# Kernel optimization log

Hardware: AMD Instinct MI355X
Metric: run time of the kernel (lower is better)

The kernel has to match this reference:

```python
import jax, jax.numpy as jnp
import numpy as np

NUM_HEADS = 4
OUTPUT_DIM = 64


def setup_inputs() -> dict:
    key = jax.random.key(0)
    k1, k2, k3 = jax.random.split(key, 3)
    B, N, F = 8, 2048, 256
    features = jax.random.normal(k1, (B, N, F), dtype=jnp.float32)
    adj_matrix = jax.random.uniform(k2, (B, N, N), dtype=jnp.float32)
    # learned params (glorot-ish scale)
    kernel = jax.random.normal(k3, (F, OUTPUT_DIM * NUM_HEADS), dtype=jnp.float32) * (1.0 / np.sqrt(F))
    bias = jnp.zeros((OUTPUT_DIM * NUM_HEADS,), dtype=jnp.float32)
    return {"features": features, "adj_matrix": adj_matrix, "kernel": kernel, "bias": bias}


def reference(features, adj_matrix, kernel, bias):
    B, N, F = features.shape
    H, D = NUM_HEADS, OUTPUT_DIM
    Wh = jnp.matmul(features, kernel)                 # [B, N, H*D]
    Whh = Wh.reshape(B, N, H, D)                      # [B, N, H, D]
    # per-node, per-head score: inner product Wh1 @ Wh2 = ||Wh||^2
    e = jnp.sum(Whh * Whh, axis=-1)                   # [B, N, H]
    attention = jax.nn.softmax(e, axis=1)             # softmax over nodes
    attention = jnp.mean(attention, axis=2)           # head mean -> [B, N]
    # adjacency mask (broadcast column score over neighbors)
    A = attention[:, :, None] * adj_matrix            # [B, N, N]
    out = jnp.matmul(A, Wh) + bias                    # [B, N, H*D]
    return jax.nn.relu(out)
```

## Files before the change

kernel.cpp:

```cpp
#include <hip/hip_runtime.h>
#include <hip/hip_bf16.h>

#define BATCH 8
#define NNODE 2048
#define FDIM 256
#define HD 256
#define NH 4
#define MROWS (BATCH*NNODE)

typedef float f32x4 __attribute__((ext_vector_type(4)));
typedef short s16x8 __attribute__((ext_vector_type(8)));
typedef unsigned short ushort_t;

#define MFMA __builtin_amdgcn_mfma_f32_16x16x32_bf16
#define SCHED0() __builtin_amdgcn_sched_barrier(0)
#define SBAR() __builtin_amdgcn_s_barrier()

__device__ __forceinline__ ushort_t f2bf(float f) {
    unsigned u = __builtin_bit_cast(unsigned, f);
    u += 0x7fffu + ((u >> 16) & 1u);
    return (ushort_t)(u >> 16);
}
__device__ __forceinline__ void split2(float f, ushort_t& h, ushort_t& l) {
    unsigned u = __builtin_bit_cast(unsigned, f);
    h = (ushort_t)(u >> 16);
    float fh = __builtin_bit_cast(float, u & 0xffff0000u);
    float lo = f - fh;
    l = (ushort_t)(__builtin_bit_cast(unsigned, lo) >> 16);
}

#define GLOAD16(gp, lp) __builtin_amdgcn_global_load_lds( \
    (const __attribute__((address_space(1))) void*)(gp),  \
    (__attribute__((address_space(3))) void*)(lp), 16, 0, 0)

__global__ __launch_bounds__(256) void wprep_kernel(
    const float* __restrict__ Wm,
    ushort_t* __restrict__ wt_hi, ushort_t* __restrict__ wt_lo)
{
    const int nn = blockIdx.x, k = threadIdx.x;
    ushort_t h, l;
    split2(Wm[(size_t)k * HD + nn], h, l);
    wt_hi[nn * FDIM + k] = h;
    wt_lo[nn * FDIM + k] = l;
}

__global__ __launch_bounds__(256, 4) void gemm1_kernel(
    const float* __restrict__ features,
    const ushort_t* __restrict__ wt_hi,
    const ushort_t* __restrict__ wt_lo,
    ushort_t* __restrict__ WhT_hi,
    float* __restrict__ e_out)
{
    __shared__ __align__(16) ushort_t Ah[64 * 64];
    __shared__ __align__(16) ushort_t Al[64 * 64];
    __shared__ __align__(16) ushort_t Bh[64 * 64];
    __shared__ __align__(16) ushort_t Bl[64 * 64];
    __shared__ float red[64][2];

    const int tid = threadIdx.x, lane = tid & 63, w = tid >> 6;
    const int wr = w >> 1, wc = w & 1;
    const int row0 = blockIdx.x * 64;
    const int head = blockIdx.y;
    const int col0 = head * 64;

    const float* Ab = features + (size_t)row0 * FDIM;
    const ushort_t* Bhg = wt_hi + (size_t)col0 * FDIM;
    const ushort_t* Blg = wt_lo + (size_t)col0 * FDIM;

    const int sr0 = tid >> 3;
    const int sg8 = tid & 7;
    const int bc = (lane >> 3);
    const int bs = lane & 7;

    f32x4 ar[4];
    f32x4 acc[2][2];
    #pragma unroll
    for (int m = 0; m < 2; ++m)
        #pragma unroll
        for (int n = 0; n < 2; ++n) acc[m][n] = (f32x4)0.f;

    #define G1_LOADA(K0) do {                                                  \
        _Pragma("unroll")                                                      \
        for (int i = 0; i < 2; ++i) {                                          \
            const int r = sr0 + 32 * i;                                        \
            ar[2*i]   = *(const f32x4*)&Ab[(size_t)r * FDIM + (K0) + sg8 * 8]; \
            ar[2*i+1] = *(const f32x4*)&Ab[(size_t)r * FDIM + (K0) + sg8 * 8 + 4]; \
        }                                                                      \
    } while (0)

    #define G1_STAGEA() do {                                                   \
        _Pragma("unroll")                                                      \
        for (int i = 0; i < 2; ++i) {                                          \
            const int r = sr0 + 32 * i;                                        \
            s16x8 vh, vl; ushort_t hh, ll;                                     \
            _Pragma("unroll")                                                  \
            for (int j = 0; j < 4; ++j) {                                      \
                split2(ar[2*i][j], hh, ll);  vh[j] = (short)hh; vl[j] = (short)ll; \
            }                                                                  \
            _Pragma("unroll")                                                  \
            for (int j = 0; j < 4; ++j) {                                      \
                split2(ar[2*i+1][j], hh, ll); vh[4+j] = (short)hh; vl[4+j] = (short)ll; \
            }                                                                  \
            const int off = r * 64 + ((sg8 ^ (r & 7)) << 3);                   \
            *(s16x8*)&Ah[off] = vh; *(s16x8*)&Al[off] = vl;                    \
        }                                                                      \
    } while (0)

    #define G1_STAGEB(K0) do {                                                 \
        _Pragma("unroll")                                                      \
        for (int qq = 0; qq < 2; ++qq) {                                       \
            const int q = w + qq * 4;                                          \
            const int c = q * 8 + bc;                                          \
            const int g = bs ^ (c & 7);                                        \
            GLOAD16(&Bhg[(size_t)c * FDIM + (K0) + g * 8], &Bh[q * 512]);      \
            GLOAD16(&Blg[(size_t)c * FDIM + (K0) + g * 8], &Bl[q * 512]);      \
        }                                                                      \
    } while (0)

    G1_LOADA(0);
    for (int t = 0; t < 4; ++t) {
        G1_STAGEB(t * 64);
        G1_STAGEA();
        if (t < 3) G1_LOADA((t + 1) * 64);
        if (t < 3) { asm volatile("s_waitcnt lgkmcnt(0) vmcnt(4)" ::: "memory"); }
        else       { asm volatile("s_waitcnt lgkmcnt(0) vmcnt(0)" ::: "memory"); }
        SCHED0(); SBAR(); SCHED0();
        #pragma unroll
        for (int kh = 0; kh < 2; ++kh) {
            const int kg = kh * 4 + (lane >> 4);
            s16x8 afh[2], afl[2], bfh[2], bfl[2];
            #pragma unroll
            for (int m = 0; m < 2; ++m) {
                const int r = wr * 32 + m * 16 + (lane & 15);
                const int off = r * 64 + ((kg ^ (r & 7)) << 3);
                afh[m] = *(const s16x8*)&Ah[off];
                afl[m] = *(const s16x8*)&Al[off];
            }
            #pragma unroll
            for (int n = 0; n < 2; ++n) {
                const int c = wc * 32 + n * 16 + (lane & 15);
                const int off = c * 64 + ((kg ^ (c & 7)) << 3);
                bfh[n] = *(const s16x8*)&Bh[off];
                bfl[n] = *(const s16x8*)&Bl[off];
            }
            #pragma unroll
            for (int m = 0; m < 2; ++m)
                #pragma unroll
                for (int n = 0; n < 2; ++n) {
                    acc[m][n] = MFMA(afh[m], bfh[n], acc[m][n], 0, 0, 0);
                    acc[m][n] = MFMA(afh[m], bfl[n], acc[m][n], 0, 0, 0);
                    acc[m][n] = MFMA(afl[m], bfh[n], acc[m][n], 0, 0, 0);
                }
        }
        SCHED0(); SBAR(); SCHED0();
    }

    #pragma unroll
    for (int m = 0; m < 2; ++m)
        #pragma unroll
        for (int j = 0; j < 4; ++j) {
            float p = acc[m][0][j] * acc[m][0][j] + acc[m][1][j] * acc[m][1][j];
            p += __shfl_xor(p, 1, 64);
            p += __shfl_xor(p, 2, 64);
            p += __shfl_xor(p, 4, 64);
            p += __shfl_xor(p, 8, 64);
            if ((lane & 15) == 0)
                red[wr * 32 + m * 16 + (lane >> 4) * 4 + j][wc] = p;
        }

    __syncthreads();
    ushort_t* Th = Ah;
    #pragma unroll
    for (int m = 0; m < 2; ++m)
        #pragma unroll
        for (int n = 0; n < 2; ++n)
            #pragma unroll
            for (int j = 0; j < 4; ++j) {
                const int rr = wr * 32 + m * 16 + (lane >> 4) * 4 + j;
                const int cc = wc * 32 + n * 16 + (lane & 15);
                const int ad = cc * 64 + ((((rr >> 3) ^ (cc & 7))) << 3) + (rr & 7);
                Th[ad] = f2bf(acc[m][n][j]);
            }
    __syncthreads();

    if (tid < 64) {
        const int rg = row0 + tid;
        e_out[((size_t)((rg >> 11) * NH + head)) * NNODE + (rg & 2047)] =
            red[tid][0] + red[tid][1];
    }
    const int bb = row0 >> 11, node0 = row0 & 2047;
    {
        const int gid = tid + 256 * 0;
        #pragma unroll
        for (int i = 0; i < 2; ++i) {
            const int g2 = gid + 256 * i;
            const int c = g2 >> 3, gr = g2 & 7;
            const int ad = c * 64 + ((gr ^ (c & 7)) << 3);
            uint4 vh = *(const uint4*)&Th[ad];
            const size_t o = ((size_t)bb * HD + col0 + c) * NNODE + node0 + gr * 8;
            *(uint4*)&WhT_hi[o] = vh;
        }
    }
}

__global__ __launch_bounds__(256) void sm_kernel(
    const float* __restrict__ e, float* __restrict__ ms)
{
    __shared__ float red[8];
    const int bh = blockIdx.x, tid = threadIdx.x;
    const int lane = tid & 63, w = tid >> 6;
    const float* row = e + (size_t)bh * NNODE;
    float mx = -3.0e38f;
    for (int n = tid; n < NNODE; n += 256) mx = fmaxf(mx, row[n]);
    #pragma unroll
    for (int off = 32; off; off >>= 1) mx = fmaxf(mx, __shfl_xor(mx, off, 64));
    if (lane == 0) red[w] = mx;
    __syncthreads();
    mx = fmaxf(fmaxf(red[0], red[1]), fmaxf(red[2], red[3]));
    float s = 0.f;
    for (int n = tid; n < NNODE; n += 256) s += expf(row[n] - mx);
    #pragma unroll
    for (int off = 32; off; off >>= 1) s += __shfl_xor(s, off, 64);
    if (lane == 0) red[4 + w] = s;
    __syncthreads();
    if (tid == 0) {
        ms[bh * 2] = mx;
        ms[bh * 2 + 1] = 1.0f / (red[4] + red[5] + red[6] + red[7]);
    }
}

__global__ __launch_bounds__(256, 2) void gemm2_kernel(
    const float* __restrict__ adj,
    const ushort_t* __restrict__ WhT_hi,
    const float* __restrict__ e,
    const float* __restrict__ ms,
    const float* __restrict__ bias,
    float* __restrict__ out)
{
    __shared__ __align__(16) ushort_t Bh[4][64 * 64];

    const int tid = threadIdx.x, lane = tid & 63, w = tid >> 6;

    const int bid = blockIdx.x;
    const int wg = (bid & 7) * 64 + (bid >> 3);
    const int bx = wg & 15, by = (wg >> 4) & 3, b = wg >> 6;
    const int row0 = bx * 128, col0 = by * 64;

    const ushort_t* Bhg = WhT_hi + ((size_t)b * HD + col0) * NNODE;
    const float* pA = adj + (size_t)b * NNODE * NNODE
                    + (size_t)(row0 + w * 32 + (lane & 15)) * NNODE
                    + ((lane >> 4) * 8);

    const int bc = lane >> 3, bs = lane & 7;

    f32x4 arE[8], arO[8];
    s16x8 afh[2][2];
    f32x4 acc[2][4];
    #pragma unroll
    for (int m = 0; m < 2; ++m)
        #pragma unroll
        for (int n = 0; n < 4; ++n) acc[m][n] = (f32x4)0.f;

    #define G2_LOADA(AR, K0) do {                                               \
        _Pragma("unroll")                                                       \
        for (int m = 0; m < 2; ++m)                                             \
        _Pragma("unroll")                                                       \
        for (int ks = 0; ks < 2; ++ks) {                                        \
            AR[m*4+ks*2+0] = *(const f32x4*)&pA[(size_t)m * 16 * NNODE + (K0) + ks * 32]; \
            AR[m*4+ks*2+1] = *(const f32x4*)&pA[(size_t)m * 16 * NNODE + (K0) + ks * 32 + 4]; \
        }                                                                       \
    } while (0)

    #define G2_CONVERT(AR) do {                                                 \
        _Pragma("unroll")                                                       \
        for (int m = 0; m < 2; ++m)                                             \
        _Pragma("unroll")                                                       \
        for (int ks = 0; ks < 2; ++ks)                                          \
        _Pragma("unroll")                                                       \
        for (int h2 = 0; h2 < 2; ++h2)                                          \
        _Pragma("unroll")                                                       \
        for (int j = 0; j < 4; ++j)                                             \
            afh[m][ks][h2 * 4 + j] = (short)f2bf(AR[m*4+ks*2+h2][j]);           \
    } while (0)

    #define G2_STAGEB(BUF, K0) do {                                             \
        _Pragma("unroll")                                                       \
        for (int qq = 0; qq < 2; ++qq) {                                        \
            const int q = w + qq * 4;                                           \
            const int c = q * 8 + bc;                                           \
            const int g = bs ^ (c & 7);                                         \
            GLOAD16(&Bhg[(size_t)c * NNODE + (K0) + g * 8], &Bh[BUF][q * 512]); \
        }                                                                       \
    } while (0)

    #define G2_COMPUTE(BUF) do {                                                \
        _Pragma("unroll")                                                       \
        for (int ks = 0; ks < 2; ++ks) {                                        \
            const int kg = ks * 4 + (lane >> 4);                                \
            s16x8 bfh[4];                                                       \
            _Pragma("unroll")                                                   \
            for (int n = 0; n < 4; ++n) {                                       \
                const int c = n * 16 + (lane & 15);                             \
                const int off = c * 64 + ((kg ^ (c & 7)) << 3);                 \
                bfh[n] = *(const s16x8*)&Bh[BUF][off];                          \
            }                                                                   \
            __builtin_amdgcn_s_setprio(1);                                      \
            _Pragma("unroll")                                                   \
            for (int m = 0; m < 2; ++m)                                         \
            _Pragma("unroll")                                                   \
            for (int n = 0; n < 4; ++n)                                         \
                acc[m][n] = MFMA(afh[m][ks], bfh[n], acc[m][n], 0, 0, 0);       \
            __builtin_amdgcn_s_setprio(0);                                      \
        }                                                                       \
    } while (0)

    #define G2_TILE(AR, CBUF, SBUF, KC, DO_STAGE) do {                          \
        if (DO_STAGE) G2_STAGEB(SBUF, (KC) + 128);                              \
        G2_CONVERT(AR);                                                         \
        if (DO_STAGE) G2_LOADA(AR, (KC) + 128);                                 \
        asm volatile("s_waitcnt vmcnt(20)" ::: "memory");                       \
        SCHED0(); SBAR(); SCHED0();                                             \
        G2_COMPUTE(CBUF);                                                       \
    } while (0)

    G2_STAGEB(0, 0);
    G2_LOADA(arE, 0);
    G2_STAGEB(1, 64);
    G2_LOADA(arO, 64);

    #pragma unroll 1
    for (int t = 0; t < 28; t += 4) {
        G2_TILE(arE, 0, 2, t * 64, true);
        G2_TILE(arO, 1, 3, (t + 1) * 64, true);
        G2_TILE(arE, 2, 0, (t + 2) * 64, true);
        G2_TILE(arO, 3, 1, (t + 3) * 64, true);
    }
    G2_TILE(arE, 0, 2, 28 * 64, true);
    G2_TILE(arO, 1, 3, 29 * 64, true);
    G2_TILE(arE, 2, 0, 30 * 64, false);
    G2_TILE(arO, 3, 0, 31 * 64, false);

    float msm[NH], msi[NH];
    #pragma unroll
    for (int h = 0; h < NH; ++h) {
        msm[h] = ms[(b * NH + h) * 2];
        msi[h] = ms[(b * NH + h) * 2 + 1];
    }
    float rowatt[2][4];
    #pragma unroll
    for (int m = 0; m < 2; ++m)
        #pragma unroll
        for (int j = 0; j < 4; ++j) {
            const int row = row0 + w * 32 + m * 16 + (lane >> 4) * 4 + j;
            float a = 0.f;
            #pragma unroll
            for (int h = 0; h < NH; ++h)
                a += expf(e[((size_t)b * NH + h) * NNODE + row] - msm[h]) * msi[h];
            rowatt[m][j] = 0.25f * a;
        }
    #pragma unroll
    for (int n = 0; n < 4; ++n) {
        const int c = col0 + n * 16 + (lane & 15);
        const float bv = bias[c];
        #pragma unroll
        for (int m = 0; m < 2; ++m)
            #pragma unroll
            for (int j = 0; j < 4; ++j) {
                const int row = row0 + w * 32 + m * 16 + (lane >> 4) * 4 + j;
                out[((size_t)b * NNODE + row) * HD + c] =
                    fmaxf(fmaf(acc[m][n][j], rowatt[m][j], bv), 0.f);
            }
    }
}

extern "C" void kernel_launch(void* const* d_in, const int* in_sizes, int n_in,
                              void* d_out, int out_size, void* d_ws, size_t ws_size,
                              hipStream_t stream) {
    const float* features = (const float*)d_in[0];
    const float* adj      = (const float*)d_in[1];
    const float* Wm       = (const float*)d_in[2];
    const float* bias     = (const float*)d_in[3];
    float* out = (float*)d_out;

    ushort_t* WhT_hi = (ushort_t*)d_ws;
    ushort_t* wt_hi  = WhT_hi + (size_t)BATCH * HD * NNODE;
    ushort_t* wt_lo  = wt_hi + FDIM * HD;
    float* e  = (float*)(wt_lo + FDIM * HD);
    float* ms = e + (size_t)BATCH * NH * NNODE;

    wprep_kernel<<<HD, 256, 0, stream>>>(Wm, wt_hi, wt_lo);
    gemm1_kernel<<<dim3(MROWS / 64, NH), 256, 0, stream>>>(
        features, wt_hi, wt_lo, WhT_hi, e);
    sm_kernel<<<BATCH * NH, 256, 0, stream>>>(e, ms);
    gemm2_kernel<<<512, 256, 0, stream>>>(
        adj, WhT_hi, e, ms, bias, out);
}
```

Before: 265.4 us.

## Give each wave a private B buffer in gemm2 to drop block barriers

Each wave of gemm2 now stages the full 64x64 B tile into its own private double-buffered LDS slot and then reads only that slot. The s_barrier between stages goes away, replaced by per-wave waitcnt on vmcnt and lgkmcnt, and the pipeline changes from four shared buffers to two private ones. In exchange, global B traffic per block rises fourfold (each wave loads all 64 columns), LDS use doubles to 64KB, and the prefetch distance for B shrinks. A small cleanup to the epilogue loop of the first kernel is also included.

```diff
diff --git a/kernel.cpp b/kernel.cpp
--- a/kernel.cpp
+++ b/kernel.cpp
@@ -189,17 +189,14 @@
             red[tid][0] + red[tid][1];
     }
     const int bb = row0 >> 11, node0 = row0 & 2047;
-    {
-        const int gid = tid + 256 * 0;
-        #pragma unroll
-        for (int i = 0; i < 2; ++i) {
-            const int g2 = gid + 256 * i;
-            const int c = g2 >> 3, gr = g2 & 7;
-            const int ad = c * 64 + ((gr ^ (c & 7)) << 3);
-            uint4 vh = *(const uint4*)&Th[ad];
-            const size_t o = ((size_t)bb * HD + col0 + c) * NNODE + node0 + gr * 8;
-            *(uint4*)&WhT_hi[o] = vh;
-        }
+    #pragma unroll
+    for (int i = 0; i < 2; ++i) {
+        const int g2 = tid + 256 * i;
+        const int c = g2 >> 3, gr = g2 & 7;
+        const int ad = c * 64 + ((gr ^ (c & 7)) << 3);
+        uint4 vh = *(const uint4*)&Th[ad];
+        const size_t o = ((size_t)bb * HD + col0 + c) * NNODE + node0 + gr * 8;
+        *(uint4*)&WhT_hi[o] = vh;
     }
 }
 
@@ -237,7 +234,7 @@
     const float* __restrict__ bias,
     float* __restrict__ out)
 {
-    __shared__ __align__(16) ushort_t Bh[4][64 * 64];
+    __shared__ __align__(16) ushort_t Bh[4][2][64 * 64];
 
     const int tid = threadIdx.x, lane = tid & 63, w = tid >> 6;
 
@@ -251,7 +248,10 @@
                     + (size_t)(row0 + w * 32 + (lane & 15)) * NNODE
                     + ((lane >> 4) * 8);
 
-    const int bc = lane >> 3, bs = lane & 7;
+    const int scol = lane >> 3;
+    const int sgr  = (lane & 7) ^ scol;
+    ushort_t* myB0 = &Bh[w][0][0];
+    ushort_t* myB1 = &Bh[w][1][0];
 
     f32x4 arE[8], arO[8];
     s16x8 afh[2][2];
@@ -283,17 +283,15 @@
             afh[m][ks][h2 * 4 + j] = (short)f2bf(AR[m*4+ks*2+h2][j]);           \
     } while (0)
 
-    #define G2_STAGEB(BUF, K0) do {                                             \
-        _Pragma("unroll")                                                       \
-        for (int qq = 0; qq < 2; ++qq) {                                        \
-            const int q = w + qq * 4;                                           \
-            const int c = q * 8 + bc;                                           \
-            const int g = bs ^ (c & 7);                                         \
-            GLOAD16(&Bhg[(size_t)c * NNODE + (K0) + g * 8], &Bh[BUF][q * 512]); \
+    #define G2_STAGEB(LB, K0) do {                                              \
+        _Pragma("unroll")                                                       \
+        for (int i = 0; i < 8; ++i) {                                           \
+            const int c = i * 8 + scol;                                         \
+            GLOAD16(&Bhg[(size_t)c * NNODE + (K0) + sgr * 8], (LB) + i * 512);  \
         }                                                                       \
     } while (0)
 
-    #define G2_COMPUTE(BUF) do {                                                \
+    #define G2_COMPUTE(LB) do {                                                 \
         _Pragma("unroll")                                                       \
         for (int ks = 0; ks < 2; ++ks) {                                        \
             const int kg = ks * 4 + (lane >> 4);                                \
@@ -302,7 +300,7 @@
             for (int n = 0; n < 4; ++n) {                                       \
                 const int c = n * 16 + (lane & 15);                             \
                 const int off = c * 64 + ((kg ^ (c & 7)) << 3);                 \
-                bfh[n] = *(const s16x8*)&Bh[BUF][off];                          \
+                bfh[n] = *(const s16x8*)&(LB)[off];                             \
             }                                                                   \
             __builtin_amdgcn_s_setprio(1);                                      \
             _Pragma("unroll")                                                   \
@@ -314,31 +312,51 @@
         }                                                                       \
     } while (0)
 
-    #define G2_TILE(AR, CBUF, SBUF, KC, DO_STAGE) do {                          \
-        if (DO_STAGE) G2_STAGEB(SBUF, (KC) + 128);                              \
-        G2_CONVERT(AR);                                                         \
-        if (DO_STAGE) G2_LOADA(AR, (KC) + 128);                                 \
-        asm volatile("s_waitcnt vmcnt(20)" ::: "memory");                       \
-        SCHED0(); SBAR(); SCHED0();                                             \
-        G2_COMPUTE(CBUF);                                                       \
-    } while (0)
-
-    G2_STAGEB(0, 0);
+    #define LGK0() asm volatile("s_waitcnt lgkmcnt(0)" ::: "memory")
+
+    G2_STAGEB(myB0, 0);
+    SCHED0();
     G2_LOADA(arE, 0);
-    G2_STAGEB(1, 64);
+    SCHED0();
     G2_LOADA(arO, 64);
+    SCHED0();
 
     #pragma unroll 1
-    for (int t = 0; t < 28; t += 4) {
-        G2_TILE(arE, 0, 2, t * 64, true);
-        G2_TILE(arO, 1, 3, (t + 1) * 64, true);
-        G2_TILE(arE, 2, 0, (t + 2) * 64, true);
-        G2_TILE(arO, 3, 1, (t + 3) * 64, true);
-    }
-    G2_TILE(arE, 0, 2, 28 * 64, true);
-    G2_TILE(arO, 1, 3, 29 * 64, true);
-    G2_TILE(arE, 2, 0, 30 * 64, false);
-    G2_TILE(arO, 3, 0, 31 * 64, false);
+    for (int t = 0; t < 30; t += 2) {
+        LGK0(); SCHED0();
+        G2_STAGEB(myB1, (t + 1) * 64);
+        SCHED0();
+        G2_CONVERT(arE);
+        SCHED0();
+        G2_LOADA(arE, (t + 2) * 64);
+        SCHED0();
+        asm volatile("s_waitcnt vmcnt(24)" ::: "memory");
+        SCHED0();
+        G2_COMPUTE(myB0);
+        LGK0(); SCHED0();
+        G2_STAGEB(myB0, (t + 2) * 64);
+        SCHED0();
+        G2_CONVERT(arO);
+        SCHED0();
+        if (t + 3 < 32) G2_LOADA(arO, (t + 3) * 64);
+        SCHED0();
+        asm volatile("s_waitcnt vmcnt(24)" ::: "memory");
+        SCHED0();
+        G2_COMPUTE(myB1);
+    }
+    LGK0(); SCHED0();
+    G2_STAGEB(myB1, 31 * 64);
+    SCHED0();
+    G2_CONVERT(arE);
+    SCHED0();
+    asm volatile("s_waitcnt vmcnt(16)" ::: "memory");
+    SCHED0();
+    G2_COMPUTE(myB0);
+    G2_CONVERT(arO);
+    SCHED0();
+    asm volatile("s_waitcnt vmcnt(0)" ::: "memory");
+    SCHED0();
+    G2_COMPUTE(myB1);
 
     float msm[NH], msi[NH];
     #pragma unroll
```

Result: slower. 272.9 us (+2.8%).
